# Optimization experiments

Hardware: AMD Instinct MI355X
Metric: run time of the kernel (lower is better)

## Reference

```python
import jax, jax.numpy as jnp
from jax import lax
import numpy as np

B, CIN, COUT, T, H, W, KH, KW = 8, 256, 256, 16, 28, 28, 3, 3


def setup_inputs() -> dict:
    key = jax.random.key(0)
    k1, k2, k3 = jax.random.split(key, 3)
    x = jax.random.normal(k1, (B, CIN, T, H, W), dtype=jnp.float32)
    alpha = jax.random.uniform(k2, (B, CIN, T, 1, 1), dtype=jnp.float32)
    # base weight, kaiming-uniform-like init, stored as [1,1,c_out,c_in,kh,kw]
    fan_in = CIN * KH * KW
    bound = 1.0 / np.sqrt(fan_in)
    weight = jax.random.uniform(k3, (1, 1, COUT, CIN, KH, KW), dtype=jnp.float32,
                                minval=-bound, maxval=bound)
    return {"x": x, "alpha": alpha, "weight": weight}


def reference(x, alpha, weight):
    # x: [b, c_in, t, h, w]; alpha: [b, c_in, t, 1, 1]; weight: [1,1,c_out,c_in,kh,kw]
    b, c_in, t, h, w = x.shape
    c_out = weight.shape[2]
    w_base = weight[0, 0]  # [c_out, c_in, kh, kw]
    # W_t = alpha_t * W_base scales only input channels (alpha broadcasts over c_out),
    # so (alpha*W) conv x == W conv (alpha*x): modulate input, then one shared conv.
    xm = x * alpha  # [b, c_in, t, h, w]
    xm = jnp.transpose(xm, (0, 2, 1, 3, 4)).reshape(b * t, c_in, h, w)
    y = lax.conv_general_dilated(
        xm, w_base,
        window_strides=(1, 1),
        padding=((1, 1), (1, 1)),
        dimension_numbers=("NCHW", "OIHW", "NCHW"),
    )  # [b*t, c_out, h, w]
    oh, ow = y.shape[-2], y.shape[-1]
    y = y.reshape(b, t, c_out, oh, ow)
    return jnp.transpose(y, (0, 2, 1, 3, 4))  # [b, c_out, t, h, w]
```

## Files before the change

kernel.cpp:

```cpp
#include <hip/hip_runtime.h>
#include <hip/hip_bf16.h>
#include <cstdint>

#define CIN   256
#define COUT  256
#define NB    8
#define NT    16
#define NH    28
#define NW    28
#define HP    30
#define WP    30

#define XM_ELEMS   ((size_t)NB * NT * HP * WP * CIN)
#define XM_BYTES   (XM_ELEMS * 2)

typedef __bf16 bf16x8 __attribute__((ext_vector_type(8)));
typedef float  f32x4  __attribute__((ext_vector_type(4)));

#define AS1 __attribute__((address_space(1)))
#define AS3 __attribute__((address_space(3)))

static __device__ __forceinline__ unsigned short f2bf(float f) {
    __hip_bfloat16 h = __float2bfloat16(f);
    return __builtin_bit_cast(unsigned short, h);
}

__global__ void modulate_kernel(const float* __restrict__ x,
                                const float* __restrict__ alpha,
                                unsigned short* __restrict__ xm) {
    const int ci = threadIdx.x;
    const int blk = blockIdx.x;
    const int hp = blk % 30;
    const int bt = blk / 30;
    unsigned short* row = xm + (size_t)(bt * 900 + hp * 30) * 256;
    if (hp == 0 || hp == 29) {
        #pragma unroll
        for (int wp = 0; wp < 30; ++wp) row[wp * 256 + ci] = 0;
        return;
    }
    const int t = bt & 15, b = bt >> 4;
    const int h = hp - 1;
    const float a = alpha[(b * CIN + ci) * NT + t];
    const float* xrow = x + ((size_t)((b * CIN + ci) * NT + t) * NH + h) * NW;
    row[ci] = 0;
    row[29 * 256 + ci] = 0;
    const float4* xv = (const float4*)xrow;
    #pragma unroll
    for (int q = 0; q < 7; ++q) {
        float4 v = xv[q];
        row[(q * 4 + 1) * 256 + ci] = f2bf(v.x * a);
        row[(q * 4 + 2) * 256 + ci] = f2bf(v.y * a);
        row[(q * 4 + 3) * 256 + ci] = f2bf(v.z * a);
        row[(q * 4 + 4) * 256 + ci] = f2bf(v.w * a);
    }
}

__global__ void repack_w_kernel(const float* __restrict__ w,
                                unsigned short* __restrict__ wB) {
    const int ci = threadIdx.x;
    const int tap = blockIdx.x >> 8;
    const int co  = blockIdx.x & 255;
    wB[((tap * 256 + co) * 256) + ci] = f2bf(w[(co * 256 + ci) * 9 + tap]);
}


#define BAR()    __builtin_amdgcn_s_barrier()
#define LGKM0()  asm volatile("s_waitcnt lgkmcnt(0)" ::: "memory")
#define VMW(N)   asm volatile("s_waitcnt vmcnt(" #N ")" ::: "memory")
#define SCHED0() __builtin_amdgcn_sched_barrier(0)
#define PRIO(x)  __builtin_amdgcn_s_setprio(x)

#define STAGE_F(P) do {                                                       \
    const int kh2 = (tapS * 11) >> 5;                                         \
    const int kw2 = tapS - 3 * kh2;                                           \
    const int aOff = tapS * 65536 + cicS * 32;                                \
    const int bOff = ((kh2 - 1) * 30 + (kw2 - 1)) * 256 + cicS * 32;          \
    _Pragma("unroll") for (int c_ = 0; c_ < 2; ++c_)                          \
        __builtin_amdgcn_global_load_lds(                                     \
            (const AS1 void*)(aSrc + aOff + c_ * 32768),                      \
            (AS3 void*)(lds + (P)*32768 + (c_*128 + wave*16)*64 + lane*16),   \
            16, 0, 0);                                                        \
    _Pragma("unroll") for (int c_ = 0; c_ < 2; ++c_)                          \
        __builtin_amdgcn_global_load_lds(                                     \
            (const AS1 void*)(bL[c_] + bOff),                                 \
            (AS3 void*)(lds + (P)*32768 + 16384 + (c_*128 + wave*16)*64 + lane*16), \
            16, 0, 0);                                                        \
    if (++tapS == 9) { tapS = 0; ++cicS; }                                    \
} while (0)

#define READF(S, P) do {                                                      \
    _Pragma("unroll") for (int m_ = 0; m_ < 4; ++m_)                          \
        fa##S[m_] = *(const bf16x8*)(lds + (P)*32768 +                        \
            (wm*64 + m_*16 + l15)*64 + readSwz);                              \
    _Pragma("unroll") for (int f_ = 0; f_ < NF; ++f_)                         \
        fb##S[f_] = *(const bf16x8*)(lds + (P)*32768 + 16384 +                \
            (wn*(NF*16) + f_*16 + l15)*64 + readSwz);                         \
} while (0)

#define MFMA_T(S) do {                                                        \
    _Pragma("unroll") for (int m_ = 0; m_ < 4; ++m_)                          \
    _Pragma("unroll") for (int f_ = 0; f_ < NF; ++f_)                         \
        acc[m_][f_] = __builtin_amdgcn_mfma_f32_16x16x32_bf16(                \
            fb##S[f_], fa##S[m_], acc[m_][f_], 0, 0, 0);                      \
} while (0)

#define BODY_S(CS, NS, NBUF, SBUF) do {                                       \
    VMW(4);                                                                   \
    SCHED0();                                                                 \
    BAR();                                                                    \
    READF(NS, NBUF);                                                          \
    STAGE_F(SBUF);                                                            \
    SCHED0();                                                                 \
    PRIO(1); MFMA_T(CS); PRIO(0);                                             \
    LGKM0();                                                                  \
    SCHED0();                                                                 \
} while (0)

#define BODY_N(CS, NS, NBUF, VMN) do {                                        \
    VMW(VMN);                                                                 \
    SCHED0();                                                                 \
    BAR();                                                                    \
    READF(NS, NBUF);                                                          \
    SCHED0();                                                                 \
    PRIO(1); MFMA_T(CS); PRIO(0);                                             \
    LGKM0();                                                                  \
    SCHED0();                                                                 \
} while (0)

template<int NF>
__device__ __forceinline__ void conv_body(
    const unsigned short* __restrict__ xm,
    const unsigned short* __restrict__ wB,
    float* __restrict__ out,
    char* lds, const int n0)
{
    const int tid  = threadIdx.x;
    const int wave = tid >> 6;
    const int lane = tid & 63;
    const int l15  = lane & 15;
    const int wm   = wave >> 1;
    const int wn   = wave & 1;
    const int BN   = NF * 32;

    const int swzE = 8 * ((lane & 3) ^ ((lane >> 3) & 3));
    const unsigned short* aSrc = wB + (wave * 16 + (lane >> 2)) * 256 + swzE;

    const unsigned short* bL[2];
    #pragma unroll
    for (int c_ = 0; c_ < 2; ++c_) {
        int nl = c_ * 128 + wave * 16 + (lane >> 2);
        nl = nl > BN - 1 ? BN - 1 : nl;
        const int n  = n0 + nl;
        const int w_ = n % 28, h_ = (n / 28) % 28, bt = n / 784;
        bL[c_] = xm + (size_t)((bt * 30 + h_ + 1) * 30 + (w_ + 1)) * 256 + swzE;
    }

    const int readSwz = ((lane >> 4) ^ ((l15 >> 1) & 3)) << 4;

    f32x4 acc[4][NF];
    #pragma unroll
    for (int i = 0; i < 4; ++i)
        #pragma unroll
        for (int j = 0; j < NF; ++j) acc[i][j] = f32x4{0.f, 0.f, 0.f, 0.f};

    bf16x8 faA[4], fbA[NF], faB[4], fbB[NF];

    int tapS = 0, cicS = 0;
    STAGE_F(0);
    STAGE_F(1);
    STAGE_F(2);
    VMW(8);
    SCHED0();
    BAR();
    READF(A, 0);
    LGKM0();
    SCHED0();

    #pragma unroll 1
    for (int it = 0; it < 11; ++it) {
        BODY_S(A, B, 1, 0);
        BODY_S(B, A, 2, 1);
        BODY_S(A, B, 0, 2);
        BODY_S(B, A, 1, 0);
        BODY_S(A, B, 2, 1);
        BODY_S(B, A, 0, 2);
    }
    BODY_S(A, B, 1, 0);
    BODY_S(B, A, 2, 1);
    BODY_S(A, B, 0, 2);
    BODY_N(B, A, 1, 4);
    BODY_N(A, B, 2, 0);
    PRIO(1); MFMA_T(B); PRIO(0);

    #pragma unroll
    for (int f = 0; f < NF; ++f) {
        const int n  = n0 + wn * (NF * 16) + f * 16 + ((lane >> 4) << 2);
        const int bt = n / 784;
        const int hw = n - bt * 784;
        const int b = bt >> 4, t = bt & 15;
        float* obase = out + ((size_t)(b * 256) * 16 + t) * 784 + hw;
        #pragma unroll
        for (int m = 0; m < 4; ++m) {
            const int co = wm * 64 + m * 16 + l15;
            *(f32x4*)(obase + (size_t)co * 12544) = acc[m][f];
        }
    }
}

__global__ __launch_bounds__(512, 2) void conv_gemm_kernel(
    const unsigned short* __restrict__ xm,
    const unsigned short* __restrict__ wB,
    float* __restrict__ out) {
    __shared__ __align__(1024) char lds[98304];
    const int bx = blockIdx.x;
    if (bx < 64) {
        conv_body<7>(xm, wB, out, lds, bx * 224);
    } else {
        conv_body<6>(xm, wB, out, lds, 14336 + (bx - 64) * 192);
    }
}

extern "C" void kernel_launch(void* const* d_in, const int* in_sizes, int n_in,
                              void* d_out, int out_size, void* d_ws, size_t ws_size,
                              hipStream_t stream) {
    const float* x      = (const float*)d_in[0];
    const float* alpha  = (const float*)d_in[1];
    const float* weight = (const float*)d_in[2];
    float* out = (float*)d_out;

    unsigned short* xm = (unsigned short*)d_ws;
    unsigned short* wB = (unsigned short*)((char*)d_ws + XM_BYTES);

    modulate_kernel<<<dim3(NB * NT * HP), dim3(256), 0, stream>>>(x, alpha, xm);
    repack_w_kernel<<<dim3(9 * 256), dim3(256), 0, stream>>>(weight, wB);
    conv_gemm_kernel<<<dim3(512), dim3(512), 0, stream>>>(xm, wB, out);
}
```

Baseline: 156.8 us.

## Warp-specialize conv GEMM with dedicated producer waves and 4-stage LDS ring

Splits each block into 8 compute waves and 2 producer waves. The producer waves issue all global-to-LDS copies into a 4-deep ring buffer, while the compute waves only read LDS and run MFMAs, synchronising through block barriers. The goal is to take load issue and vmcnt waits off the MFMA waves so copies overlap compute more fully. In exchange LDS grows to 128KB and launch bounds drop to one 640-thread block per CU, which lowers occupancy compared with the previous two blocks per CU.

```diff
diff --git a/kernel.cpp b/kernel.cpp
--- a/kernel.cpp
+++ b/kernel.cpp
@@ -70,24 +70,6 @@
 #define SCHED0() __builtin_amdgcn_sched_barrier(0)
 #define PRIO(x)  __builtin_amdgcn_s_setprio(x)
 
-#define STAGE_F(P) do {                                                       \
-    const int kh2 = (tapS * 11) >> 5;                                         \
-    const int kw2 = tapS - 3 * kh2;                                           \
-    const int aOff = tapS * 65536 + cicS * 32;                                \
-    const int bOff = ((kh2 - 1) * 30 + (kw2 - 1)) * 256 + cicS * 32;          \
-    _Pragma("unroll") for (int c_ = 0; c_ < 2; ++c_)                          \
-        __builtin_amdgcn_global_load_lds(                                     \
-            (const AS1 void*)(aSrc + aOff + c_ * 32768),                      \
-            (AS3 void*)(lds + (P)*32768 + (c_*128 + wave*16)*64 + lane*16),   \
-            16, 0, 0);                                                        \
-    _Pragma("unroll") for (int c_ = 0; c_ < 2; ++c_)                          \
-        __builtin_amdgcn_global_load_lds(                                     \
-            (const AS1 void*)(bL[c_] + bOff),                                 \
-            (AS3 void*)(lds + (P)*32768 + 16384 + (c_*128 + wave*16)*64 + lane*16), \
-            16, 0, 0);                                                        \
-    if (++tapS == 9) { tapS = 0; ++cicS; }                                    \
-} while (0)
-
 #define READF(S, P) do {                                                      \
     _Pragma("unroll") for (int m_ = 0; m_ < 4; ++m_)                          \
         fa##S[m_] = *(const bf16x8*)(lds + (P)*32768 +                        \
@@ -104,119 +86,135 @@
             fb##S[f_], fa##S[m_], acc[m_][f_], 0, 0, 0);                      \
 } while (0)
 
-#define BODY_S(CS, NS, NBUF, SBUF) do {                                       \
-    VMW(4);                                                                   \
-    SCHED0();                                                                 \
+#define CBODY(CS, NS, NB) do {                                                \
     BAR();                                                                    \
-    READF(NS, NBUF);                                                          \
-    STAGE_F(SBUF);                                                            \
+    READF(NS, NB);                                                            \
     SCHED0();                                                                 \
     PRIO(1); MFMA_T(CS); PRIO(0);                                             \
     LGKM0();                                                                  \
     SCHED0();                                                                 \
 } while (0)
 
-#define BODY_N(CS, NS, NBUF, VMN) do {                                        \
-    VMW(VMN);                                                                 \
-    SCHED0();                                                                 \
-    BAR();                                                                    \
-    READF(NS, NBUF);                                                          \
-    SCHED0();                                                                 \
-    PRIO(1); MFMA_T(CS); PRIO(0);                                             \
-    LGKM0();                                                                  \
-    SCHED0();                                                                 \
+#define STAGEP(P) do {                                                        \
+    const int kh2 = (tapS * 11) >> 5;                                         \
+    const int kw2 = tapS - 3 * kh2;                                           \
+    const int aOff = tapS * 65536 + cicS * 32;                                \
+    const int bOff = ((kh2 - 1) * 30 + (kw2 - 1)) * 256 + cicS * 32;          \
+    char* dst_ = lds + (size_t)(P) * 32768;                                   \
+    _Pragma("unroll") for (int i_ = 0; i_ < 8; ++i_)                          \
+        __builtin_amdgcn_global_load_lds(                                     \
+            (const AS1 void*)(aB[i_] + aOff),                                 \
+            (AS3 void*)(dst_ + (pw8 + i_) * 1024 + lane * 16), 16, 0, 0);     \
+    _Pragma("unroll") for (int i_ = 0; i_ < 8; ++i_)                          \
+        __builtin_amdgcn_global_load_lds(                                     \
+            (const AS1 void*)(bB[i_] + bOff),                                 \
+            (AS3 void*)(dst_ + 16384 + (pw8 + i_) * 1024 + lane * 16), 16, 0, 0); \
+    if (++tapS == 9) { tapS = 0; ++cicS; }                                    \
 } while (0)
 
 template<int NF>
-__device__ __forceinline__ void conv_body(
+__device__ __forceinline__ void run_block(
     const unsigned short* __restrict__ xm,
     const unsigned short* __restrict__ wB,
     float* __restrict__ out,
     char* lds, const int n0)
 {
-    const int tid  = threadIdx.x;
-    const int wave = tid >> 6;
-    const int lane = tid & 63;
-    const int l15  = lane & 15;
-    const int wm   = wave >> 1;
-    const int wn   = wave & 1;
-    const int BN   = NF * 32;
-
-    const int swzE = 8 * ((lane & 3) ^ ((lane >> 3) & 3));
-    const unsigned short* aSrc = wB + (wave * 16 + (lane >> 2)) * 256 + swzE;
-
-    const unsigned short* bL[2];
-    #pragma unroll
-    for (int c_ = 0; c_ < 2; ++c_) {
-        int nl = c_ * 128 + wave * 16 + (lane >> 2);
-        nl = nl > BN - 1 ? BN - 1 : nl;
-        const int n  = n0 + nl;
-        const int w_ = n % 28, h_ = (n / 28) % 28, bt = n / 784;
-        bL[c_] = xm + (size_t)((bt * 30 + h_ + 1) * 30 + (w_ + 1)) * 256 + swzE;
-    }
-
-    const int readSwz = ((lane >> 4) ^ ((l15 >> 1) & 3)) << 4;
-
-    f32x4 acc[4][NF];
-    #pragma unroll
-    for (int i = 0; i < 4; ++i)
-        #pragma unroll
-        for (int j = 0; j < NF; ++j) acc[i][j] = f32x4{0.f, 0.f, 0.f, 0.f};
-
-    bf16x8 faA[4], fbA[NF], faB[4], fbB[NF];
-
-    int tapS = 0, cicS = 0;
-    STAGE_F(0);
-    STAGE_F(1);
-    STAGE_F(2);
-    VMW(8);
-    SCHED0();
-    BAR();
-    READF(A, 0);
-    LGKM0();
-    SCHED0();
-
-    #pragma unroll 1
-    for (int it = 0; it < 11; ++it) {
-        BODY_S(A, B, 1, 0);
-        BODY_S(B, A, 2, 1);
-        BODY_S(A, B, 0, 2);
-        BODY_S(B, A, 1, 0);
-        BODY_S(A, B, 2, 1);
-        BODY_S(B, A, 0, 2);
-    }
-    BODY_S(A, B, 1, 0);
-    BODY_S(B, A, 2, 1);
-    BODY_S(A, B, 0, 2);
-    BODY_N(B, A, 1, 4);
-    BODY_N(A, B, 2, 0);
-    PRIO(1); MFMA_T(B); PRIO(0);
-
-    #pragma unroll
-    for (int f = 0; f < NF; ++f) {
-        const int n  = n0 + wn * (NF * 16) + f * 16 + ((lane >> 4) << 2);
-        const int bt = n / 784;
-        const int hw = n - bt * 784;
-        const int b = bt >> 4, t = bt & 15;
-        float* obase = out + ((size_t)(b * 256) * 16 + t) * 784 + hw;
-        #pragma unroll
-        for (int m = 0; m < 4; ++m) {
-            const int co = wm * 64 + m * 16 + l15;
-            *(f32x4*)(obase + (size_t)co * 12544) = acc[m][f];
-        }
-    }
-}
-
-__global__ __launch_bounds__(512, 2) void conv_gemm_kernel(
+    const int tid = threadIdx.x;
+    if (tid < 512) {
+        const int wave = tid >> 6;
+        const int lane = tid & 63;
+        const int l15  = lane & 15;
+        const int wm   = wave >> 1;
+        const int wn   = wave & 1;
+        const int readSwz = ((lane >> 4) ^ ((l15 >> 1) & 3)) << 4;
+
+        f32x4 acc[4][NF];
+        #pragma unroll
+        for (int i = 0; i < 4; ++i)
+            #pragma unroll
+            for (int j = 0; j < NF; ++j) acc[i][j] = f32x4{0.f, 0.f, 0.f, 0.f};
+
+        bf16x8 faA[4], fbA[NF], faB[4], fbB[NF];
+
+        BAR();
+        READF(A, 0);
+        LGKM0();
+        SCHED0();
+
+        #pragma unroll 1
+        for (int it = 0; it < 17; ++it) {
+            CBODY(A, B, 1);
+            CBODY(B, A, 2);
+            CBODY(A, B, 3);
+            CBODY(B, A, 0);
+        }
+        CBODY(A, B, 1);
+        CBODY(B, A, 2);
+        CBODY(A, B, 3);
+        PRIO(1); MFMA_T(B); PRIO(0);
+
+        #pragma unroll
+        for (int f = 0; f < NF; ++f) {
+            const int n  = n0 + wn * (NF * 16) + f * 16 + ((lane >> 4) << 2);
+            const int bt = n / 784;
+            const int hw = n - bt * 784;
+            const int b = bt >> 4, t = bt & 15;
+            float* obase = out + ((size_t)(b * 256) * 16 + t) * 784 + hw;
+            #pragma unroll
+            for (int m = 0; m < 4; ++m) {
+                const int co = wm * 64 + m * 16 + l15;
+                *(f32x4*)(obase + (size_t)co * 12544) = acc[m][f];
+            }
+        }
+    } else {
+        const int ptid = tid - 512;
+        const int pw   = ptid >> 6;
+        const int lane = ptid & 63;
+        const int pw8  = pw * 8;
+        const int BN   = NF * 32;
+        const int swzE = 8 * ((lane & 3) ^ ((lane >> 3) & 3));
+
+        const unsigned short* aB[8];
+        const unsigned short* bB[8];
+        #pragma unroll
+        for (int i = 0; i < 8; ++i) {
+            const int row = (pw8 + i) * 16 + (lane >> 2);
+            aB[i] = wB + row * 256 + swzE;
+            int nl = row > BN - 1 ? BN - 1 : row;
+            const int n  = n0 + nl;
+            const int w_ = n % 28, h_ = (n / 28) % 28, bt = n / 784;
+            bB[i] = xm + (size_t)((bt * 30 + h_ + 1) * 30 + (w_ + 1)) * 256 + swzE;
+        }
+
+        int tapS = 0, cicS = 0;
+        STAGEP(0);
+        STAGEP(1);
+        STAGEP(2);
+        VMW(32);
+        BAR();
+        #pragma unroll 1
+        for (int k = 1; k <= 69; ++k) {
+            STAGEP((k + 2) & 3);
+            VMW(32);
+            BAR();
+        }
+        VMW(16);
+        BAR();
+        VMW(0);
+        BAR();
+    }
+}
+
+__global__ __launch_bounds__(640, 1) void conv_gemm_kernel(
     const unsigned short* __restrict__ xm,
     const unsigned short* __restrict__ wB,
     float* __restrict__ out) {
-    __shared__ __align__(1024) char lds[98304];
+    __shared__ __align__(1024) char lds[131072];
     const int bx = blockIdx.x;
     if (bx < 64) {
-        conv_body<7>(xm, wB, out, lds, bx * 224);
+        run_block<7>(xm, wB, out, lds, bx * 224);
     } else {
-        conv_body<6>(xm, wB, out, lds, 14336 + (bx - 64) * 192);
+        run_block<6>(xm, wB, out, lds, 14336 + (bx - 64) * 192);
     }
 }
 
@@ -233,5 +231,5 @@
 
     modulate_kernel<<<dim3(NB * NT * HP), dim3(256), 0, stream>>>(x, alpha, xm);
     repack_w_kernel<<<dim3(9 * 256), dim3(256), 0, stream>>>(weight, wB);
-    conv_gemm_kernel<<<dim3(512), dim3(512), 0, stream>>>(xm, wB, out);
-}
+    conv_gemm_kernel<<<dim3(512), dim3(640), 0, stream>>>(xm, wB, out);
+}
```

New measurement: 506.3 us. 223% more time.
